# Performance work log

Hardware: AMD Instinct MI355X
Metric: run time of the kernel (lower is better)

The kernel has to match this reference:

```python
import jax, jax.numpy as jnp
import numpy as np

E = 1280   # embed_dim
H = 16     # num_heads
D = E // H # head_dim = 80
S = 3072   # total tokens


def _rotate_half(x):
    x1, x2 = x[..., : D // 2], x[..., D // 2:]
    return jnp.concatenate((-x2, x1), axis=-1)


def setup_inputs() -> dict:
    key = jax.random.key(0)
    ks = jax.random.split(key, 7)
    x = jax.random.normal(ks[0], (S, E), dtype=jnp.float32)
    # rotary embeddings: cos/sin of random angles, shape (S, head_dim)
    ang = jax.random.uniform(ks[1], (S, D), dtype=jnp.float32) * (2 * np.pi)
    cos = jnp.cos(ang)
    sin = jnp.sin(ang)
    # 8 variable-length segments covering all S tokens
    cu_seqlens = jnp.array([0, 256, 640, 1024, 1536, 1920, 2304, 2688, 3072], dtype=jnp.int32)
    qkv_w = jax.random.normal(ks[2], (3 * E, E), dtype=jnp.float32) * 0.02
    qkv_b = jax.random.normal(ks[3], (3 * E,), dtype=jnp.float32) * 0.02
    proj_w = jax.random.normal(ks[4], (E, E), dtype=jnp.float32) * 0.02
    proj_b = jax.random.normal(ks[5], (E,), dtype=jnp.float32) * 0.02
    return {"x": x, "cu_seqlens": cu_seqlens, "cos": cos, "sin": sin,
            "qkv_w": qkv_w, "qkv_b": qkv_b, "proj_w": proj_w, "proj_b": proj_b}


def reference(x, cu_seqlens, cos, sin, qkv_w, qkv_b, proj_w, proj_b):
    # QKV projection: (S, 3E)
    qkv = x @ qkv_w.T + qkv_b
    q, k, v = jnp.split(qkv, 3, axis=-1)
    q = q.reshape(S, H, D)
    k = k.reshape(S, H, D)
    v = v.reshape(S, H, D)
    # inline RoPE, broadcast over heads (cos/sin: (S,1,D))
    c = cos[:, None, :]
    s = sin[:, None, :]
    q = q * c + _rotate_half(q) * s
    k = k * c + _rotate_half(k) * s
    # block-diagonal varlen attention: tokens attend only within their segment
    seg_ids = jnp.searchsorted(cu_seqlens, jnp.arange(S), side="right")  # (S,)
    mask = seg_ids[:, None] == seg_ids[None, :]                           # (S,S)
    scale = 1.0 / jnp.sqrt(jnp.asarray(D, dtype=q.dtype))
    scores = jnp.einsum("qhd,khd->hqk", q, k) * scale                    # (H,S,S)
    neg = jnp.finfo(scores.dtype).min
    scores = jnp.where(mask[None, :, :], scores, neg)
    attn = jax.nn.softmax(scores, axis=-1)
    out = jnp.einsum("hqk,khd->qhd", attn, v).reshape(S, E)
    return out @ proj_w.T + proj_b
```

## Files before the change

### kernel.cpp

```cpp
#include <hip/hip_runtime.h>
#include <hip/hip_bf16.h>

#define S_LEN 3072
#define E_DIM 1280
#define NH 16
#define HD 80
#define HDP 96
#define QKV_N 3840

typedef unsigned short u16;
typedef unsigned int u32;
typedef __bf16 bf16x8 __attribute__((ext_vector_type(8)));
typedef float f32x4 __attribute__((ext_vector_type(4)));

__device__ __forceinline__ u16 bf16_bits(float f) {
  __hip_bfloat16 b = __float2bfloat16(f);
  return *reinterpret_cast<u16*>(&b);
}
__device__ __forceinline__ float bf16_to_f(u16 u) {
  unsigned int x = ((unsigned int)u) << 16;
  return __uint_as_float(x);
}
__device__ __forceinline__ void gload_lds16(const u16* g, u16* l) {
  __builtin_amdgcn_global_load_lds(
      (const __attribute__((address_space(1))) void*)g,
      (__attribute__((address_space(3))) void*)l, 16, 0, 0);
}
__device__ __forceinline__ int imin(int a, int b) { return a < b ? a : b; }

#define XB_F4    983040
#define WQKV_F4  1228800
#define WPROJ_F4 409600
__global__ __launch_bounds__(256) void f32_to_bf16_3(const float* __restrict__ sx,
                                                     const float* __restrict__ sq,
                                                     const float* __restrict__ sp,
                                                     u16* __restrict__ dst) {
  int i = blockIdx.x * 256 + threadIdx.x;
  float4 v;
  if (i < XB_F4) v = reinterpret_cast<const float4*>(sx)[i];
  else if (i < XB_F4 + WQKV_F4) v = reinterpret_cast<const float4*>(sq)[i - XB_F4];
  else v = reinterpret_cast<const float4*>(sp)[i - XB_F4 - WQKV_F4];
  ushort4 o;
  o.x = bf16_bits(v.x); o.y = bf16_bits(v.y); o.z = bf16_bits(v.z); o.w = bf16_bits(v.w);
  reinterpret_cast<ushort4*>(dst)[i] = o;
}

template<int OUT_F32>
__global__ __launch_bounds__(256) void gemm_nt(const u16* __restrict__ A,
                                               const u16* __restrict__ B,
                                               const float* __restrict__ bias,
                                               void* __restrict__ Cout,
                                               int M, int N, int K, int nbx) {
  __shared__ u16 As[128 * 64];
  __shared__ u16 Bs[128 * 64];
  const int t = threadIdx.x;
  const int lane = t & 63;
  const int wave = t >> 6;
  const int l15 = lane & 15, l4 = lane >> 4;
  const int wm = (wave >> 1) * 64, wn = (wave & 1) * 64;

  const int nwg = gridDim.x;
  const int lg = (blockIdx.x & 7) * (nwg >> 3) + (blockIdx.x >> 3);
  const int m0 = (lg / nbx) * 128, n0 = (lg % nbx) * 128;

  const u16* gA[4];
  const u16* gB[4];
  u16* lA[4];
  u16* lB[4];
  #pragma unroll
  for (int i = 0; i < 4; ++i) {
    const int c = i * 256 + t;
    const int row = c >> 3;
    const int col = ((c & 7) ^ (row & 7)) * 8;
    gA[i] = A + (size_t)(m0 + row) * K + col;
    gB[i] = B + (size_t)(n0 + row) * K + col;
    lA[i] = &As[c * 8];
    lB[i] = &Bs[c * 8];
  }

  int aoff[4][2], boff[4][2];
  #pragma unroll
  for (int i = 0; i < 4; ++i)
    #pragma unroll
    for (int kk = 0; kk < 2; ++kk) {
      aoff[i][kk] = (wm + i * 16 + l15) * 64 + ((kk * 4 + l4) ^ (l15 & 7)) * 8;
      boff[i][kk] = (wn + i * 16 + l15) * 64 + ((kk * 4 + l4) ^ (l15 & 7)) * 8;
    }

  f32x4 acc[4][4] = {};

  const int nk = K >> 6;
  for (int kt = 0; kt < nk; ++kt) {
    const int k0 = kt << 6;
    #pragma unroll
    for (int i = 0; i < 4; ++i) gload_lds16(gA[i] + k0, lA[i]);
    #pragma unroll
    for (int i = 0; i < 4; ++i) gload_lds16(gB[i] + k0, lB[i]);
    __syncthreads();
    bf16x8 af[4][2], bfr[4][2];
    #pragma unroll
    for (int i = 0; i < 4; ++i)
      #pragma unroll
      for (int kk = 0; kk < 2; ++kk) {
        af[i][kk]  = *reinterpret_cast<const bf16x8*>(&As[aoff[i][kk]]);
        bfr[i][kk] = *reinterpret_cast<const bf16x8*>(&Bs[boff[i][kk]]);
      }
    __builtin_amdgcn_s_setprio(1);
    #pragma unroll
    for (int kk = 0; kk < 2; ++kk)
      #pragma unroll
      for (int i = 0; i < 4; ++i)
        #pragma unroll
        for (int j = 0; j < 4; ++j)
          acc[i][j] = __builtin_amdgcn_mfma_f32_16x16x32_bf16(af[i][kk], bfr[j][kk],
                                                              acc[i][j], 0, 0, 0);
    __builtin_amdgcn_s_setprio(0);
    __syncthreads();
  }

  #pragma unroll
  for (int i = 0; i < 4; ++i) {
    #pragma unroll
    for (int j = 0; j < 4; ++j) {
      const int col = n0 + wn + j * 16 + l15;
      const float bv = bias[col];
      const int rowb = m0 + wm + i * 16 + l4 * 4;
      #pragma unroll
      for (int r = 0; r < 4; ++r) {
        float v = acc[i][j][r] + bv;
        if (OUT_F32)
          reinterpret_cast<float*>(Cout)[(size_t)(rowb + r) * N + col] = v;
        else
          reinterpret_cast<u16*>(Cout)[(size_t)(rowb + r) * N + col] = bf16_bits(v);
      }
    }
  }
}

__global__ __launch_bounds__(256) void rope_scatter(const u16* __restrict__ qkv,
                                                    const float* __restrict__ cosb,
                                                    const float* __restrict__ sinb,
                                                    u16* __restrict__ qp,
                                                    u16* __restrict__ kp) {
  const int t = threadIdx.x;
  const int sl = t >> 6;
  const int p = t & 63;
  const int s = blockIdx.x * 4 + sl;
  const int h = blockIdx.y;
  const size_t ib = (size_t)s * QKV_N + h * HD;
  const size_t ob = ((size_t)h * S_LEN + s) * HDP;
  if (p < 40) {
    const float scale = 0.1118033988749895f;
    float q1 = bf16_to_f(qkv[ib + p]);
    float q2 = bf16_to_f(qkv[ib + 40 + p]);
    float k1 = bf16_to_f(qkv[ib + E_DIM + p]);
    float k2 = bf16_to_f(qkv[ib + E_DIM + 40 + p]);
    float c1 = cosb[(size_t)s * HD + p],      s1 = sinb[(size_t)s * HD + p];
    float c2 = cosb[(size_t)s * HD + 40 + p], s2 = sinb[(size_t)s * HD + 40 + p];
    qp[ob + p]      = bf16_bits((q1 * c1 - q2 * s1) * scale);
    qp[ob + 40 + p] = bf16_bits((q2 * c2 + q1 * s2) * scale);
    kp[ob + p]      = bf16_bits(k1 * c1 - k2 * s1);
    kp[ob + 40 + p] = bf16_bits(k2 * c2 + k1 * s2);
  } else if (p < 48) {
    const int pd = HD + (p - 40) * 2;
    qp[ob + pd] = 0; qp[ob + pd + 1] = 0;
    kp[ob + pd] = 0; kp[ob + pd + 1] = 0;
  }
}

__global__ __launch_bounds__(256) void v_transpose(const u16* __restrict__ qkv,
                                                   u16* __restrict__ vt) {
  const int idx = blockIdx.x * 256 + threadIdx.x;
  const int d = idx % HD;
  const int h = (idx / HD) % NH;
  const int sb = idx / (HD * NH);
  const int s0 = sb * 8;
  if (s0 >= S_LEN) return;
  u16 b[8];
  #pragma unroll
  for (int j = 0; j < 8; ++j)
    b[j] = qkv[(size_t)(s0 + j) * QKV_N + 2 * E_DIM + h * HD + d];
  uint4 pk;
  pk.x = b[0] | ((unsigned)b[1] << 16);
  pk.y = b[2] | ((unsigned)b[3] << 16);
  pk.z = b[4] | ((unsigned)b[5] << 16);
  pk.w = b[6] | ((unsigned)b[7] << 16);
  *reinterpret_cast<uint4*>(&vt[((size_t)h * HD + d) * S_LEN + s0]) = pk;
}

__global__ __launch_bounds__(256) void attn_fwd(const u16* __restrict__ qp,
                                                const u16* __restrict__ kp,
                                                const u16* __restrict__ vt,
                                                const int* __restrict__ cu, int ncu,
                                                u16* __restrict__ ao) {
  __shared__ u16 Ks[2][64][104];
  __shared__ u16 Pl[4][16][72];

  const int lg = ((blockIdx.x & 7) * 96) + (blockIdx.x >> 3);
  const int h = lg / 48;
  const int q0 = (lg % 48) * 64;

  const int t = threadIdx.x;
  const int wave = t >> 6;
  const int lane = t & 63;
  const int l15 = lane & 15, l4 = lane >> 4;
  const int qr = q0 + wave * 16;

  int lo = 0, hi = S_LEN;
  for (int i = 0; i + 1 < ncu; ++i) {
    int a = cu[i], b = cu[i + 1];
    if (q0 >= a && q0 < b) { lo = a; hi = b; }
  }
  const int nt = (hi - lo + 63) >> 6;

  const u16* qh = qp + (size_t)h * S_LEN * HDP;
  const u16* kh = kp + (size_t)h * S_LEN * HDP;
  const u16* vh = vt + (size_t)h * HD * S_LEN;

  bf16x8 qf[3];
  #pragma unroll
  for (int c = 0; c < 3; ++c)
    qf[c] = *reinterpret_cast<const bf16x8*>(&qh[(size_t)(qr + l15) * HDP + c * 32 + l4 * 8]);

  {
    bf16x8 kreg[3];
    #pragma unroll
    for (int i = 0; i < 3; ++i) {
      const int c2 = i * 256 + t;
      const int r = c2 / 12, cc = c2 % 12;
      const int row = imin(lo + r, S_LEN - 1);
      kreg[i] = *reinterpret_cast<const bf16x8*>(&kh[(size_t)row * HDP + cc * 8]);
    }
    #pragma unroll
    for (int i = 0; i < 3; ++i) {
      const int c2 = i * 256 + t;
      const int r = c2 / 12, cc = c2 % 12;
      *reinterpret_cast<bf16x8*>(&Ks[0][r][cc * 8]) = kreg[i];
    }
    __syncthreads();
  }

  f32x4 oacc[5] = {};
  float mrow = -INFINITY, lrow = 0.f;
  const float L2E = 1.4426950408889634f;

  int pwr[4];
  #pragma unroll
  for (int f = 0; f < 4; ++f)
    pwr[f] = ((f * 2 + (l4 >> 1)) ^ (l15 & 7)) * 8 + (l4 & 1) * 4;
  int prd[2];
  #pragma unroll
  for (int kc = 0; kc < 2; ++kc)
    prd[kc] = ((kc * 4 + l4) ^ (l15 & 7)) * 8;

  int cur = 0;
  for (int ti = 0; ti < nt; ++ti) {
    const int kb = lo + ti * 64;
    const int kbL = imin(kb, S_LEN - 64);

    bf16x8 vreg[2][5];
    #pragma unroll
    for (int kc = 0; kc < 2; ++kc)
      #pragma unroll
      for (int df = 0; df < 5; ++df)
        vreg[kc][df] = *reinterpret_cast<const bf16x8*>(
            &vh[(size_t)(df * 16 + l15) * S_LEN + kbL + kc * 32 + l4 * 8]);

    const bool more = (ti + 1) < nt;
    bf16x8 kreg[3];
    if (more) {
      const int kb2 = lo + (ti + 1) * 64;
      #pragma unroll
      for (int i = 0; i < 3; ++i) {
        const int c2 = i * 256 + t;
        const int r = c2 / 12, cc = c2 % 12;
        const int row = imin(kb2 + r, S_LEN - 1);
        kreg[i] = *reinterpret_cast<const bf16x8*>(&kh[(size_t)row * HDP + cc * 8]);
      }
    }

    f32x4 sc[4];
    #pragma unroll
    for (int f = 0; f < 4; ++f) { f32x4 z = {0.f, 0.f, 0.f, 0.f}; sc[f] = z; }
    __builtin_amdgcn_s_setprio(1);
    #pragma unroll
    for (int f = 0; f < 4; ++f)
      #pragma unroll
      for (int c = 0; c < 3; ++c) {
        bf16x8 kf = *reinterpret_cast<const bf16x8*>(&Ks[cur][f * 16 + l15][c * 32 + l4 * 8]);
        sc[f] = __builtin_amdgcn_mfma_f32_16x16x32_bf16(kf, qf[c], sc[f], 0, 0, 0);
      }
    __builtin_amdgcn_s_setprio(0);

    if (kb + 64 > hi) {
      #pragma unroll
      for (int f = 0; f < 4; ++f)
        #pragma unroll
        for (int r = 0; r < 4; ++r)
          if (kb + f * 16 + l4 * 4 + r >= hi) sc[f][r] = -INFINITY;
    }

    float tm = -INFINITY;
    #pragma unroll
    for (int f = 0; f < 4; ++f)
      #pragma unroll
      for (int r = 0; r < 4; ++r) tm = fmaxf(tm, sc[f][r]);
    tm = fmaxf(tm, __shfl_xor(tm, 16, 64));
    tm = fmaxf(tm, __shfl_xor(tm, 32, 64));

    if (__any(tm > mrow + 8.f)) {
      float mn = fmaxf(mrow, tm);
      float corr = exp2f((mrow - mn) * L2E);
      mrow = mn;
      lrow *= corr;
      #pragma unroll
      for (int df = 0; df < 5; ++df)
        #pragma unroll
        for (int r = 0; r < 4; ++r) oacc[df][r] *= corr;
    }

    float rs = 0.f;
    #pragma unroll
    for (int f = 0; f < 4; ++f) {
      float p0 = exp2f((sc[f][0] - mrow) * L2E);
      float p1 = exp2f((sc[f][1] - mrow) * L2E);
      float p2 = exp2f((sc[f][2] - mrow) * L2E);
      float p3 = exp2f((sc[f][3] - mrow) * L2E);
      rs += (p0 + p1) + (p2 + p3);
      uint2 w;
      w.x = (u32)bf16_bits(p0) | ((u32)bf16_bits(p1) << 16);
      w.y = (u32)bf16_bits(p2) | ((u32)bf16_bits(p3) << 16);
      *reinterpret_cast<uint2*>(&Pl[wave][l15][pwr[f]]) = w;
    }
    rs += __shfl_xor(rs, 16, 64);
    rs += __shfl_xor(rs, 32, 64);
    lrow += rs;

    asm volatile("s_waitcnt lgkmcnt(0)" ::: "memory");

    __builtin_amdgcn_s_setprio(1);
    #pragma unroll
    for (int kc = 0; kc < 2; ++kc) {
      bf16x8 pf = *reinterpret_cast<const bf16x8*>(&Pl[wave][l15][prd[kc]]);
      #pragma unroll
      for (int df = 0; df < 5; ++df)
        oacc[df] = __builtin_amdgcn_mfma_f32_16x16x32_bf16(vreg[kc][df], pf, oacc[df], 0, 0, 0);
    }
    __builtin_amdgcn_s_setprio(0);

    if (more) {
      #pragma unroll
      for (int i = 0; i < 3; ++i) {
        const int c2 = i * 256 + t;
        const int r = c2 / 12, cc = c2 % 12;
        *reinterpret_cast<bf16x8*>(&Ks[cur ^ 1][r][cc * 8]) = kreg[i];
      }
    }
    __syncthreads();
    cur ^= 1;
  }

  const float inv = 1.0f / lrow;
  #pragma unroll
  for (int df = 0; df < 5; ++df) {
    ushort4 o;
    o.x = bf16_bits(oacc[df][0] * inv);
    o.y = bf16_bits(oacc[df][1] * inv);
    o.z = bf16_bits(oacc[df][2] * inv);
    o.w = bf16_bits(oacc[df][3] * inv);
    *reinterpret_cast<ushort4*>(
        &ao[(size_t)(qr + l15) * E_DIM + h * HD + df * 16 + l4 * 4]) = o;
  }
}

extern "C" void kernel_launch(void* const* d_in, const int* in_sizes, int n_in,
                              void* d_out, int out_size, void* d_ws, size_t ws_size,
                              hipStream_t stream) {
  const float* x      = (const float*)d_in[0];
  const int*   cu     = (const int*)d_in[1];
  const float* cosb   = (const float*)d_in[2];
  const float* sinb   = (const float*)d_in[3];
  const float* qkv_w  = (const float*)d_in[4];
  const float* qkv_b  = (const float*)d_in[5];
  const float* proj_w = (const float*)d_in[6];
  const float* proj_b = (const float*)d_in[7];
  float* out = (float*)d_out;

  u16* xb     = (u16*)d_ws;
  u16* wqkvb  = xb     + (size_t)S_LEN * E_DIM;
  u16* wprojb = wqkvb  + (size_t)3 * E_DIM * E_DIM;
  u16* qkv    = wprojb + (size_t)E_DIM * E_DIM;
  u16* qp     = qkv    + (size_t)S_LEN * QKV_N;
  u16* kp     = qp     + (size_t)NH * S_LEN * HDP;
  u16* vt     = kp     + (size_t)NH * S_LEN * HDP;
  u16* attn   = vt     + (size_t)NH * HD * S_LEN;

  const int nf4 = XB_F4 + WQKV_F4 + WPROJ_F4;
  f32_to_bf16_3<<<nf4 / 256, 256, 0, stream>>>(x, qkv_w, proj_w, xb);

  gemm_nt<0><<<(QKV_N / 128) * (S_LEN / 128), 256, 0, stream>>>(
      xb, wqkvb, qkv_b, qkv, S_LEN, QKV_N, E_DIM, QKV_N / 128);

  rope_scatter<<<dim3(S_LEN / 4, NH), 256, 0, stream>>>(qkv, cosb, sinb, qp, kp);
  v_transpose<<<(NH * HD * (S_LEN / 8)) / 256, 256, 0, stream>>>(qkv, vt);

  attn_fwd<<<NH * (S_LEN / 64), 256, 0, stream>>>(qp, kp, vt, cu, in_sizes[1], attn);

  gemm_nt<1><<<(E_DIM / 128) * (S_LEN / 128), 256, 0, stream>>>(
      attn, wprojb, proj_b, out, S_LEN, E_DIM, E_DIM, E_DIM / 128);
}
```

Baseline: 122.2 us.

## Merge RoPE and V-transpose kernels; read K fragments directly from global in attention

Merges the RoPE scatter and V-transpose kernels into one launch that dispatches on block index, removing one kernel launch and its gap. In the attention kernel, the LDS double-buffered K tile, its staging loads and the per-iteration __syncthreads are removed; each wave now loads its K MFMA fragments straight from global memory. This drops the shared-memory traffic and barriers, but leans on L2/cache for K reuse across the four waves and exposes global latency in the QK^T loop. The out-of-range clamps on K and V rows are also removed, which relies on segment ends being multiples of 64.

```diff
diff --git a/kernel.cpp b/kernel.cpp
--- a/kernel.cpp
+++ b/kernel.cpp
@@ -137,55 +137,58 @@
   }
 }
 
-__global__ __launch_bounds__(256) void rope_scatter(const u16* __restrict__ qkv,
-                                                    const float* __restrict__ cosb,
-                                                    const float* __restrict__ sinb,
-                                                    u16* __restrict__ qp,
-                                                    u16* __restrict__ kp) {
+#define ROPE_NB 12288
+#define VT_NB   1920
+__global__ __launch_bounds__(256) void rope_vt(const u16* __restrict__ qkv,
+                                               const float* __restrict__ cosb,
+                                               const float* __restrict__ sinb,
+                                               u16* __restrict__ qp,
+                                               u16* __restrict__ kp,
+                                               u16* __restrict__ vt) {
+  const int b = blockIdx.x;
   const int t = threadIdx.x;
-  const int sl = t >> 6;
-  const int p = t & 63;
-  const int s = blockIdx.x * 4 + sl;
-  const int h = blockIdx.y;
-  const size_t ib = (size_t)s * QKV_N + h * HD;
-  const size_t ob = ((size_t)h * S_LEN + s) * HDP;
-  if (p < 40) {
-    const float scale = 0.1118033988749895f;
-    float q1 = bf16_to_f(qkv[ib + p]);
-    float q2 = bf16_to_f(qkv[ib + 40 + p]);
-    float k1 = bf16_to_f(qkv[ib + E_DIM + p]);
-    float k2 = bf16_to_f(qkv[ib + E_DIM + 40 + p]);
-    float c1 = cosb[(size_t)s * HD + p],      s1 = sinb[(size_t)s * HD + p];
-    float c2 = cosb[(size_t)s * HD + 40 + p], s2 = sinb[(size_t)s * HD + 40 + p];
-    qp[ob + p]      = bf16_bits((q1 * c1 - q2 * s1) * scale);
-    qp[ob + 40 + p] = bf16_bits((q2 * c2 + q1 * s2) * scale);
-    kp[ob + p]      = bf16_bits(k1 * c1 - k2 * s1);
-    kp[ob + 40 + p] = bf16_bits(k2 * c2 + k1 * s2);
-  } else if (p < 48) {
-    const int pd = HD + (p - 40) * 2;
-    qp[ob + pd] = 0; qp[ob + pd + 1] = 0;
-    kp[ob + pd] = 0; kp[ob + pd + 1] = 0;
-  }
-}
-
-__global__ __launch_bounds__(256) void v_transpose(const u16* __restrict__ qkv,
-                                                   u16* __restrict__ vt) {
-  const int idx = blockIdx.x * 256 + threadIdx.x;
-  const int d = idx % HD;
-  const int h = (idx / HD) % NH;
-  const int sb = idx / (HD * NH);
-  const int s0 = sb * 8;
-  if (s0 >= S_LEN) return;
-  u16 b[8];
-  #pragma unroll
-  for (int j = 0; j < 8; ++j)
-    b[j] = qkv[(size_t)(s0 + j) * QKV_N + 2 * E_DIM + h * HD + d];
-  uint4 pk;
-  pk.x = b[0] | ((unsigned)b[1] << 16);
-  pk.y = b[2] | ((unsigned)b[3] << 16);
-  pk.z = b[4] | ((unsigned)b[5] << 16);
-  pk.w = b[6] | ((unsigned)b[7] << 16);
-  *reinterpret_cast<uint4*>(&vt[((size_t)h * HD + d) * S_LEN + s0]) = pk;
+  if (b < ROPE_NB) {
+    const int h = b / 768;
+    const int sl = t >> 6;
+    const int p = t & 63;
+    const int s = (b % 768) * 4 + sl;
+    const size_t ib = (size_t)s * QKV_N + h * HD;
+    const size_t ob = ((size_t)h * S_LEN + s) * HDP;
+    if (p < 40) {
+      const float scale = 0.1118033988749895f;
+      float q1 = bf16_to_f(qkv[ib + p]);
+      float q2 = bf16_to_f(qkv[ib + 40 + p]);
+      float k1 = bf16_to_f(qkv[ib + E_DIM + p]);
+      float k2 = bf16_to_f(qkv[ib + E_DIM + 40 + p]);
+      float c1 = cosb[(size_t)s * HD + p],      s1 = sinb[(size_t)s * HD + p];
+      float c2 = cosb[(size_t)s * HD + 40 + p], s2 = sinb[(size_t)s * HD + 40 + p];
+      qp[ob + p]      = bf16_bits((q1 * c1 - q2 * s1) * scale);
+      qp[ob + 40 + p] = bf16_bits((q2 * c2 + q1 * s2) * scale);
+      kp[ob + p]      = bf16_bits(k1 * c1 - k2 * s1);
+      kp[ob + 40 + p] = bf16_bits(k2 * c2 + k1 * s2);
+    } else if (p < 48) {
+      const int pd = HD + (p - 40) * 2;
+      qp[ob + pd] = 0; qp[ob + pd + 1] = 0;
+      kp[ob + pd] = 0; kp[ob + pd + 1] = 0;
+    }
+  } else {
+    const int idx = (b - ROPE_NB) * 256 + t;
+    const int d = idx % HD;
+    const int h = (idx / HD) % NH;
+    const int sb = idx / (HD * NH);
+    const int s0 = sb * 8;
+    if (s0 >= S_LEN) return;
+    u16 bb[8];
+    #pragma unroll
+    for (int j = 0; j < 8; ++j)
+      bb[j] = qkv[(size_t)(s0 + j) * QKV_N + 2 * E_DIM + h * HD + d];
+    uint4 pk;
+    pk.x = bb[0] | ((unsigned)bb[1] << 16);
+    pk.y = bb[2] | ((unsigned)bb[3] << 16);
+    pk.z = bb[4] | ((unsigned)bb[5] << 16);
+    pk.w = bb[6] | ((unsigned)bb[7] << 16);
+    *reinterpret_cast<uint4*>(&vt[((size_t)h * HD + d) * S_LEN + s0]) = pk;
+  }
 }
 
 __global__ __launch_bounds__(256) void attn_fwd(const u16* __restrict__ qp,
@@ -193,7 +196,6 @@
                                                 const u16* __restrict__ vt,
                                                 const int* __restrict__ cu, int ncu,
                                                 u16* __restrict__ ao) {
-  __shared__ u16 Ks[2][64][104];
   __shared__ u16 Pl[4][16][72];
 
   const int lg = ((blockIdx.x & 7) * 96) + (blockIdx.x >> 3);
@@ -222,24 +224,6 @@
   for (int c = 0; c < 3; ++c)
     qf[c] = *reinterpret_cast<const bf16x8*>(&qh[(size_t)(qr + l15) * HDP + c * 32 + l4 * 8]);
 
-  {
-    bf16x8 kreg[3];
-    #pragma unroll
-    for (int i = 0; i < 3; ++i) {
-      const int c2 = i * 256 + t;
-      const int r = c2 / 12, cc = c2 % 12;
-      const int row = imin(lo + r, S_LEN - 1);
-      kreg[i] = *reinterpret_cast<const bf16x8*>(&kh[(size_t)row * HDP + cc * 8]);
-    }
-    #pragma unroll
-    for (int i = 0; i < 3; ++i) {
-      const int c2 = i * 256 + t;
-      const int r = c2 / 12, cc = c2 % 12;
-      *reinterpret_cast<bf16x8*>(&Ks[0][r][cc * 8]) = kreg[i];
-    }
-    __syncthreads();
-  }
-
   f32x4 oacc[5] = {};
   float mrow = -INFINITY, lrow = 0.f;
   const float L2E = 1.4426950408889634f;
@@ -253,10 +237,8 @@
   for (int kc = 0; kc < 2; ++kc)
     prd[kc] = ((kc * 4 + l4) ^ (l15 & 7)) * 8;
 
-  int cur = 0;
   for (int ti = 0; ti < nt; ++ti) {
     const int kb = lo + ti * 64;
-    const int kbL = imin(kb, S_LEN - 64);
 
     bf16x8 vreg[2][5];
     #pragma unroll
@@ -264,20 +246,7 @@
       #pragma unroll
       for (int df = 0; df < 5; ++df)
         vreg[kc][df] = *reinterpret_cast<const bf16x8*>(
-            &vh[(size_t)(df * 16 + l15) * S_LEN + kbL + kc * 32 + l4 * 8]);
-
-    const bool more = (ti + 1) < nt;
-    bf16x8 kreg[3];
-    if (more) {
-      const int kb2 = lo + (ti + 1) * 64;
-      #pragma unroll
-      for (int i = 0; i < 3; ++i) {
-        const int c2 = i * 256 + t;
-        const int r = c2 / 12, cc = c2 % 12;
-        const int row = imin(kb2 + r, S_LEN - 1);
-        kreg[i] = *reinterpret_cast<const bf16x8*>(&kh[(size_t)row * HDP + cc * 8]);
-      }
-    }
+            &vh[(size_t)(df * 16 + l15) * S_LEN + kb + kc * 32 + l4 * 8]);
 
     f32x4 sc[4];
     #pragma unroll
@@ -287,7 +256,8 @@
     for (int f = 0; f < 4; ++f)
       #pragma unroll
       for (int c = 0; c < 3; ++c) {
-        bf16x8 kf = *reinterpret_cast<const bf16x8*>(&Ks[cur][f * 16 + l15][c * 32 + l4 * 8]);
+        bf16x8 kf = *reinterpret_cast<const bf16x8*>(
+            &kh[(size_t)(kb + f * 16 + l15) * HDP + c * 32 + l4 * 8]);
         sc[f] = __builtin_amdgcn_mfma_f32_16x16x32_bf16(kf, qf[c], sc[f], 0, 0, 0);
       }
     __builtin_amdgcn_s_setprio(0);
@@ -347,17 +317,6 @@
         oacc[df] = __builtin_amdgcn_mfma_f32_16x16x32_bf16(vreg[kc][df], pf, oacc[df], 0, 0, 0);
     }
     __builtin_amdgcn_s_setprio(0);
-
-    if (more) {
-      #pragma unroll
-      for (int i = 0; i < 3; ++i) {
-        const int c2 = i * 256 + t;
-        const int r = c2 / 12, cc = c2 % 12;
-        *reinterpret_cast<bf16x8*>(&Ks[cur ^ 1][r][cc * 8]) = kreg[i];
-      }
-    }
-    __syncthreads();
-    cur ^= 1;
   }
 
   const float inv = 1.0f / lrow;
@@ -401,8 +360,7 @@
   gemm_nt<0><<<(QKV_N / 128) * (S_LEN / 128), 256, 0, stream>>>(
       xb, wqkvb, qkv_b, qkv, S_LEN, QKV_N, E_DIM, QKV_N / 128);
 
-  rope_scatter<<<dim3(S_LEN / 4, NH), 256, 0, stream>>>(qkv, cosb, sinb, qp, kp);
-  v_transpose<<<(NH * HD * (S_LEN / 8)) / 256, 256, 0, stream>>>(qkv, vt);
+  rope_vt<<<ROPE_NB + VT_NB, 256, 0, stream>>>(qkv, cosb, sinb, qp, kp, vt);
 
   attn_fwd<<<NH * (S_LEN / 64), 256, 0, stream>>>(qp, kp, vt, cu, in_sizes[1], attn);
 
```

Measured after the change: 128.9 us. +5.5%, slower.
